# Optimization experiments

Measured on AMD Instinct MI355X. Metric: run time of the kernel, lower is better.

Reference implementation:

```python
import jax, jax.numpy as jnp
import numpy as np

B, L, D, H, T = 4, 1024, 1024, 16, 64


def cubic_interp_1d(vec, coords):
    # Catmull-Rom interpolation of 1D vec at real-valued coords (any shape).
    Lv = vec.shape[0]
    i = jnp.floor(coords).astype(jnp.int32)
    t = coords - i.astype(coords.dtype)
    im1 = jnp.clip(i - 1, 0, Lv - 1)
    i0 = jnp.clip(i, 0, Lv - 1)
    i1 = jnp.clip(i + 1, 0, Lv - 1)
    i2 = jnp.clip(i + 2, 0, Lv - 1)
    p0, p1, p2, p3 = vec[im1], vec[i0], vec[i1], vec[i2]
    t2 = t * t
    t3 = t2 * t
    return 0.5 * (2 * p1 + (-p0 + p2) * t + (2 * p0 - 5 * p1 + 4 * p2 - p3) * t2
                  + (-p0 + 3 * p1 - 3 * p2 + p3) * t3)


def linear_interp_1d(vec, coords):
    Lv = vec.shape[0]
    i = jnp.floor(coords).astype(jnp.int32)
    t = coords - i.astype(coords.dtype)
    i0 = jnp.clip(i, 0, Lv - 1)
    i1 = jnp.clip(i + 1, 0, Lv - 1)
    return vec[i0] * (1 - t) + vec[i1] * t


def setup_inputs() -> dict:
    key = jax.random.key(0)
    ks = jax.random.split(key, 12)
    s = 1.0 / np.sqrt(D)
    return {
        "x": jax.random.normal(ks[0], (B, L, D), jnp.float32),
        "t_enc": jax.random.normal(ks[1], (B, L, T), jnp.float32),
        "WQ": jax.random.normal(ks[2], (D, D), jnp.float32) * s,
        "WK": jax.random.normal(ks[3], (D, D), jnp.float32) * s,
        "WV": jax.random.normal(ks[4], (D, D), jnp.float32) * s,
        "WO": jax.random.normal(ks[5], (D, D), jnp.float32) * s,
        "bO": jnp.zeros((D,), jnp.float32),
        "Wt": jax.random.normal(ks[6], (T,), jnp.float32) * (1.0 / np.sqrt(T)),
        "bt": jnp.zeros((), jnp.float32),
        "p_mat": jax.random.normal(ks[7], (D, L), jnp.float32) * 0.02,
        "r_mat": jax.random.normal(ks[8], (D, L), jnp.float32) * 0.02,
        "alpha": jnp.ones((H,), jnp.float32),
        "beta": jnp.ones((H,), jnp.float32),
        "gamma": jnp.zeros((H,), jnp.float32),
    }


def reference(x, t_enc, WQ, WK, WV, WO, bO, Wt, bt, p_mat, r_mat, alpha, beta, gamma):
    Bx, Lx, Dx = x.shape
    d = Dx // H
    # projections: torch Linear y = x @ W.T
    Q = (x @ WQ.T).reshape(Bx, Lx, H, d).transpose(0, 2, 1, 3)  # [B,H,L,d]
    K = (x @ WK.T).reshape(Bx, Lx, H, d).transpose(0, 2, 1, 3)
    V = (x @ WV.T).reshape(Bx, Lx, H, d).transpose(0, 2, 1, 3)
    P = x.reshape(Bx, Lx, H, d).transpose(0, 2, 1, 3)
    # time-warped coordinates
    tau = jax.nn.sigmoid(t_enc @ Wt + bt)          # [B,L]
    coords = tau * (Lx - 1)
    # q_sca = cubic_interp(p_mat, coords).sum(-1); interp is linear in p_mat,
    # so interpolate the d-summed vector (same math, no [B,L,d] blowup).
    q_sca = cubic_interp_1d(p_mat.sum(0), coords)  # [B,L]
    delta = jnp.abs(coords[:, :, None] - coords[:, None, :])   # [B,L,L]
    r_sca = linear_interp_1d(r_mat.sum(0), delta)              # [B,L,L]
    qsum = q_sca[:, :, None] + q_sca[:, None, :]               # [B,L,L]
    Pij = jnp.einsum('bhid,bhjd->bhij', P, P)                  # [B,H,L,L]
    a = alpha[None, :, None, None]
    b = beta[None, :, None, None]
    c = gamma[None, :, None, None]
    S = a * qsum[:, None] + b * r_sca[:, None] + c
    scores = jnp.einsum('bhid,bhjd->bhij', Q, K) / jnp.sqrt(jnp.asarray(d, x.dtype)) + S * Pij
    attn = jax.nn.softmax(scores, axis=-1)
    out = jnp.einsum('bhij,bhjd->bhid', attn, V)
    out = out.transpose(0, 2, 1, 3).reshape(Bx, Lx, Dx)
    return out @ WO.T + bO
```

## Files before the change

kernel.cpp:

```cpp
#include <hip/hip_runtime.h>
#include <cstdint>
#include <cstddef>

typedef __attribute__((ext_vector_type(8))) short s8v;
typedef __attribute__((ext_vector_type(4))) float f32x4;

__device__ __forceinline__ unsigned short f2bf(float f) {
  unsigned int u = __builtin_bit_cast(unsigned int, f);
  unsigned int r = (u + 0x7fffu + ((u >> 16) & 1u)) >> 16;
  return (unsigned short)r;
}
__device__ __forceinline__ float bf2f(unsigned short s) {
  unsigned int u = ((unsigned int)s) << 16;
  return __builtin_bit_cast(float, u);
}

__device__ __forceinline__ void gload16(const void* g, void* l) {
  __builtin_amdgcn_global_load_lds(
      (const __attribute__((address_space(1))) void*)g,
      (__attribute__((address_space(3))) void*)l, 16, 0, 0);
}


__global__ __launch_bounds__(256)
void colsum_kernel(const float* __restrict__ p_mat, const float* __restrict__ r_mat,
                   float* __restrict__ q_vec, float* __restrict__ r_vec) {
  int col = blockIdx.x * 256 + threadIdx.x;
  int d0 = blockIdx.y * 32;
  float sp = 0.f, sr = 0.f;
  for (int d = d0; d < d0 + 32; ++d) {
    sp += p_mat[d * 1024 + col];
    sr += r_mat[d * 1024 + col];
  }
  atomicAdd(&q_vec[col], sp);
  atomicAdd(&r_vec[col], sr);
}

__global__ __launch_bounds__(256)
void coords_kernel(const float* __restrict__ t_enc, const float* __restrict__ Wt,
                   const float* __restrict__ bt, const float* __restrict__ q_vec,
                   float* __restrict__ coords, float* __restrict__ q_sca) {
  int item = blockIdx.x * 4 + (threadIdx.x >> 6);
  int lane = threadIdx.x & 63;
  float v = t_enc[(size_t)item * 64 + lane] * Wt[lane];
  v += __shfl_xor(v, 32);
  v += __shfl_xor(v, 16);
  v += __shfl_xor(v, 8);
  v += __shfl_xor(v, 4);
  v += __shfl_xor(v, 2);
  v += __shfl_xor(v, 1);
  if (lane == 0) {
    float z = v + bt[0];
    float tau = 1.0f / (1.0f + expf(-z));
    float c = tau * 1023.0f;
    coords[item] = c;
    float fi = floorf(c);
    int i = (int)fi;
    float t = c - fi;
    int im1 = i - 1; if (im1 < 0) im1 = 0; if (im1 > 1023) im1 = 1023;
    int i0 = i; if (i0 < 0) i0 = 0; if (i0 > 1023) i0 = 1023;
    int i1 = i + 1; if (i1 > 1023) i1 = 1023;
    int i2 = i + 2; if (i2 > 1023) i2 = 1023;
    float p0 = q_vec[im1], p1 = q_vec[i0], p2 = q_vec[i1], p3 = q_vec[i2];
    float t2 = t * t, t3 = t2 * t;
    q_sca[item] = 0.5f * (2.f * p1 + (-p0 + p2) * t +
                          (2.f * p0 - 5.f * p1 + 4.f * p2 - p3) * t2 +
                          (-p0 + 3.f * p1 - 3.f * p2 + p3) * t3);
  }
}

__global__ __launch_bounds__(256)
void conv_all_kernel(const float* __restrict__ x,
                     const float* __restrict__ w0, const float* __restrict__ w1,
                     const float* __restrict__ w2, const float* __restrict__ w3,
                     unsigned short* __restrict__ xb, unsigned short* __restrict__ xlo,
                     unsigned short* __restrict__ wb) {
  int bx = blockIdx.x;
  if (bx < 2048) {
    size_t i8 = ((size_t)bx * 256 + threadIdx.x) * 8;
    float4 a = *(const float4*)(x + i8);
    float4 b = *(const float4*)(x + i8 + 4);
    float v[8] = {a.x, a.y, a.z, a.w, b.x, b.y, b.z, b.w};
    s8v h, lo;
    #pragma unroll
    for (int j = 0; j < 8; ++j) {
      unsigned short hh = f2bf(v[j]);
      h[j] = (short)hh;
      lo[j] = (short)f2bf(v[j] - bf2f(hh));
    }
    *(s8v*)(xb + i8) = h;
    *(s8v*)(xlo + i8) = lo;
  } else {
    size_t i8 = ((size_t)(bx - 2048) * 256 + threadIdx.x) * 8;
    int sel = (int)(i8 >> 20);
    const float* w = (sel == 0) ? w0 : (sel == 1) ? w1 : (sel == 2) ? w2 : w3;
    size_t off = i8 & 0xFFFFF;
    float4 a = *(const float4*)(w + off);
    float4 b = *(const float4*)(w + off + 4);
    float v[8] = {a.x, a.y, a.z, a.w, b.x, b.y, b.z, b.w};
    s8v h;
    #pragma unroll
    for (int j = 0; j < 8; ++j) h[j] = (short)f2bf(v[j]);
    *(s8v*)(wb + i8) = h;
  }
}


__global__ __launch_bounds__(256, 2)
void gemm_qkv_kernel(const unsigned short* __restrict__ Abuf,
                     const unsigned short* __restrict__ Wb,
                     unsigned short* __restrict__ Qb,
                     unsigned short* __restrict__ Kb,
                     unsigned short* __restrict__ Vb) {
  __shared__ unsigned short As[2][128 * 64];
  __shared__ unsigned short Bs[2][128 * 64];
  const int tid = threadIdx.x, w = tid >> 6, l = tid & 63;
  const int sel = blockIdx.x >> 3;
  const int nb = (blockIdx.x & 7) * 128;
  const int m0 = blockIdx.y * 128;
  const unsigned short* Bbuf = Wb + ((size_t)sel << 20);
  const int wr = w >> 1, wc = w & 1;
  const int ll = l & 15, lg = l >> 4;
  const int cs = (((l & 7) ^ ((l >> 3) & 7)) * 8);

  const f32x4 zero4 = {0.f, 0.f, 0.f, 0.f};
  f32x4 acc[4][4];
  #pragma unroll
  for (int i = 0; i < 4; ++i) {
    #pragma unroll
    for (int j = 0; j < 4; ++j) acc[i][j] = zero4;
  }

  auto stage = [&](int kt, int buf) {
    #pragma unroll
    for (int q = 0; q < 4; ++q) {
      const int seg = w * 4 + q;
      const int row = seg * 8 + (l >> 3);
      const int col = kt * 64 + cs;
      gload16(Abuf + (size_t)(m0 + row) * 1024 + col, &As[buf][seg * 512 + l * 8]);
      gload16(Bbuf + (size_t)(nb + row) * 1024 + col, &Bs[buf][seg * 512 + l * 8]);
    }
  };

  stage(0, 0);
  for (int kt = 0; kt < 16; ++kt) {
    __syncthreads();
    if (kt < 15) stage(kt + 1, (kt + 1) & 1);
    const int bb = kt & 1;
    #pragma unroll
    for (int ks = 0; ks < 2; ++ks) {
      const int gsw = ((ks * 4 + lg) ^ (ll & 7)) * 8;
      s8v af[4], bf[4];
      #pragma unroll
      for (int mi = 0; mi < 4; ++mi)
        af[mi] = *(const s8v*)&As[bb][(wr * 64 + mi * 16 + ll) * 64 + gsw];
      #pragma unroll
      for (int ni = 0; ni < 4; ++ni)
        bf[ni] = *(const s8v*)&Bs[bb][(wc * 64 + ni * 16 + ll) * 64 + gsw];
      #pragma unroll
      for (int mi = 0; mi < 4; ++mi) {
        #pragma unroll
        for (int ni = 0; ni < 4; ++ni)
          acc[mi][ni] = __builtin_amdgcn_mfma_f32_16x16x32_bf16(af[mi], bf[ni], acc[mi][ni], 0, 0, 0);
      }
    }
  }

  unsigned short* dst = (sel == 0) ? Qb : ((sel == 1) ? Kb : Vb);
  unsigned short* ch = &As[0][0];
  const int err = tid >> 3;
  const int ecb = tid & 7;
  #pragma unroll
  for (int mi = 0; mi < 4; ++mi) {
    __syncthreads();
    #pragma unroll
    for (int ni = 0; ni < 4; ++ni) {
      #pragma unroll
      for (int r = 0; r < 4; ++r)
        ch[(wr * 16 + lg * 4 + r) * 136 + wc * 64 + ni * 16 + ll] = f2bf(acc[mi][ni][r]);
    }
    __syncthreads();
    int m = m0 + (err >> 4) * 64 + mi * 16 + (err & 15);
    int ncol = nb + ecb * 16;
    int bb2 = m >> 10, lr = m & 1023, hh = ncol >> 6, dd = ncol & 63;
    unsigned short* gp = &dst[(((size_t)bb2 * 16 + hh) * 1024 + lr) * 64 + dd];
    *(s8v*)(gp)     = *(const s8v*)&ch[err * 136 + ecb * 16];
    *(s8v*)(gp + 8) = *(const s8v*)&ch[err * 136 + ecb * 16 + 8];
  }
}


__global__ __launch_bounds__(256, 2)
void gemm_out_kernel(const unsigned short* __restrict__ Abuf,
                     const unsigned short* __restrict__ Bbuf,
                     const float* __restrict__ bO,
                     float* __restrict__ out) {
  __shared__ unsigned short As[2][128 * 64];
  __shared__ unsigned short Bs[2][128 * 64];
  const int tid = threadIdx.x, w = tid >> 6, l = tid & 63;
  const int nb = blockIdx.x * 128;
  const int m0 = blockIdx.y * 128;
  const int wr = w >> 1, wc = w & 1;
  const int ll = l & 15, lg = l >> 4;
  const int cs = (((l & 7) ^ ((l >> 3) & 7)) * 8);

  const f32x4 zero4 = {0.f, 0.f, 0.f, 0.f};
  f32x4 acc[4][4];
  #pragma unroll
  for (int i = 0; i < 4; ++i) {
    #pragma unroll
    for (int j = 0; j < 4; ++j) acc[i][j] = zero4;
  }

  auto stage = [&](int kt, int buf) {
    #pragma unroll
    for (int q = 0; q < 4; ++q) {
      const int seg = w * 4 + q;
      const int row = seg * 8 + (l >> 3);
      const int col = kt * 64 + cs;
      gload16(Abuf + (size_t)(m0 + row) * 1024 + col, &As[buf][seg * 512 + l * 8]);
      gload16(Bbuf + (size_t)(nb + row) * 1024 + col, &Bs[buf][seg * 512 + l * 8]);
    }
  };

  stage(0, 0);
  for (int kt = 0; kt < 16; ++kt) {
    __syncthreads();
    if (kt < 15) stage(kt + 1, (kt + 1) & 1);
    const int bb = kt & 1;
    #pragma unroll
    for (int ks = 0; ks < 2; ++ks) {
      const int gsw = ((ks * 4 + lg) ^ (ll & 7)) * 8;
      s8v af[4], bf[4];
      #pragma unroll
      for (int mi = 0; mi < 4; ++mi)
        af[mi] = *(const s8v*)&As[bb][(wr * 64 + mi * 16 + ll) * 64 + gsw];
      #pragma unroll
      for (int ni = 0; ni < 4; ++ni)
        bf[ni] = *(const s8v*)&Bs[bb][(wc * 64 + ni * 16 + ll) * 64 + gsw];
      #pragma unroll
      for (int mi = 0; mi < 4; ++mi) {
        #pragma unroll
        for (int ni = 0; ni < 4; ++ni)
          acc[mi][ni] = __builtin_amdgcn_mfma_f32_16x16x32_bf16(af[mi], bf[ni], acc[mi][ni], 0, 0, 0);
      }
    }
  }

  #pragma unroll
  for (int mi = 0; mi < 4; ++mi) {
    #pragma unroll
    for (int ni = 0; ni < 4; ++ni) {
      #pragma unroll
      for (int r = 0; r < 4; ++r) {
        int m = m0 + wr * 64 + mi * 16 + (l >> 4) * 4 + r;
        int ncol = nb + wc * 64 + ni * 16 + ll;
        out[(size_t)m * 1024 + ncol] = acc[mi][ni][r] + bO[ncol];
      }
    }
  }
}


__global__ __launch_bounds__(512, 2)
void attn_kernel(const unsigned short* __restrict__ Qb,
                 const unsigned short* __restrict__ Kb,
                 const unsigned short* __restrict__ Vb,
                 const unsigned short* __restrict__ xb,
                 const unsigned short* __restrict__ xlo,
                 const float* __restrict__ coords,
                 const float* __restrict__ q_sca,
                 const float* __restrict__ r_vec,
                 const float* __restrict__ alpha,
                 const float* __restrict__ beta,
                 const float* __restrict__ gamma,
                 unsigned short* __restrict__ AO) {
  __shared__ float2 rp_s[1024];
  __shared__ unsigned short Ks[2][64 * 64];
  __shared__ unsigned short Ph[2][64 * 64];
  __shared__ unsigned short Pl[2][64 * 64];
  __shared__ unsigned short Vt[64 * 64];
  __shared__ unsigned short pbuf[8][16 * 64];

  const int tid = threadIdx.x;
  const int w = tid >> 6;
  const int l = tid & 63;
  const int gid = blockIdx.x;
  const int bh = (gid & 7) * 8 + ((gid >> 3) >> 3);
  const int xt = (gid >> 3) & 7;
  const int b = bh >> 4;
  const int h = bh & 15;
  const int iw = xt * 128 + w * 16;

  for (int t = tid; t < 1024; t += 512) {
    float r0 = r_vec[t];
    float r1 = r_vec[t < 1023 ? t + 1 : 1023];
    rp_s[t] = make_float2(r0, r1);
  }

  const float INVLN2 = 1.4426950408889634f;
  const float a_h = alpha[h] * INVLN2, b_h = beta[h] * INVLN2, c_h = gamma[h] * INVLN2;
  const int lg = l >> 4;
  const int ll = l & 15;
  const int rowg = lg * 4;
  const int akg = lg * 8;

  float aqi[4], ci[4];
  #pragma unroll
  for (int r = 0; r < 4; ++r) {
    aqi[r] = fmaf(a_h, q_sca[b * 1024 + iw + rowg + r], c_h);
    ci[r] = coords[b * 1024 + iw + rowg + r];
  }

  s8v qf[2], pih[2], pil[2];
  {
    const unsigned short* qp = Qb + ((size_t)bh * 1024 + iw + ll) * 64 + akg;
    qf[0] = *(const s8v*)(qp);
    qf[1] = *(const s8v*)(qp + 32);
    const unsigned short* xp = xb + ((size_t)b * 1024 + iw + ll) * 1024 + h * 64 + akg;
    pih[0] = *(const s8v*)(xp);
    pih[1] = *(const s8v*)(xp + 32);
    const unsigned short* xq = xlo + ((size_t)b * 1024 + iw + ll) * 1024 + h * 64 + akg;
    pil[0] = *(const s8v*)(xq);
    pil[1] = *(const s8v*)(xq + 32);
  }

  const f32x4 zero4 = {0.f, 0.f, 0.f, 0.f};
  f32x4 o[4];
  #pragma unroll
  for (int ds = 0; ds < 4; ++ds) o[ds] = zero4;
  float mrow[4], lsum[4];
  #pragma unroll
  for (int r = 0; r < 4; ++r) { mrow[r] = -3.0e38f; lsum[r] = 0.f; }

  unsigned short* pw = pbuf[w];
  const int cs = (((l & 7) ^ ((l >> 3) & 7)) * 8);
  const int srow = l >> 3;

  auto stage = [&](int j0, int buf) {
    const int row = w * 8 + srow;
    gload16(Kb + ((size_t)bh * 1024 + j0 + row) * 64 + cs, &Ks[buf][w * 512 + l * 8]);
    gload16(xb + ((size_t)b * 1024 + j0 + row) * 1024 + h * 64 + cs, &Ph[buf][w * 512 + l * 8]);
    gload16(xlo + ((size_t)b * 1024 + j0 + row) * 1024 + h * 64 + cs, &Pl[buf][w * 512 + l * 8]);
  };
  auto vload = [&](int j0) -> s8v {
    return *(const s8v*)(Vb + ((size_t)bh * 1024 + j0 + l) * 64 + w * 8);
  };
  auto vwrite = [&](const s8v& vv) {
    #pragma unroll
    for (int e = 0; e < 8; ++e) {
      const int row = w * 8 + e;
      Vt[row * 64 + (((l >> 3) ^ (row & 7)) * 8) + (l & 7)] = (unsigned short)vv[e];
    }
  };

  stage(0, 0);
  s8v vv0 = vload(0);
  stage(64, 1);
  s8v vv1 = vload(64);
  vwrite(vv0);
  __syncthreads();

#define ATTN_TILE(T, PAR, VCONS, VPROD)                                          \
  {                                                                              \
    const int j0 = (T) * 64;                                                     \
    float cj[4], aqj[4];                                                         \
    _Pragma("unroll")                                                            \
    for (int s = 0; s < 4; ++s) {                                                \
      cj[s] = coords[b * 1024 + j0 + ll + 16 * s];                               \
      aqj[s] = a_h * q_sca[b * 1024 + j0 + ll + 16 * s];                         \
    }                                                                            \
    f32x4 aqk[4], app[4];                                                        \
    _Pragma("unroll")                                                            \
    for (int s = 0; s < 4; ++s) { aqk[s] = zero4; app[s] = zero4; }              \
    _Pragma("unroll")                                                            \
    for (int ks = 0; ks < 2; ++ks) {                                             \
      _Pragma("unroll")                                                          \
      for (int s = 0; s < 4; ++s) {                                              \
        const int rb = (ll + 16 * s) * 64 + (((ks * 4 + lg) ^ (ll & 7)) * 8);    \
        s8v kf = *(const s8v*)&Ks[PAR][rb];                                      \
        s8v hf = *(const s8v*)&Ph[PAR][rb];                                      \
        s8v lf = *(const s8v*)&Pl[PAR][rb];                                      \
        aqk[s] = __builtin_amdgcn_mfma_f32_16x16x32_bf16(qf[ks], kf, aqk[s], 0, 0, 0);   \
        app[s] = __builtin_amdgcn_mfma_f32_16x16x32_bf16(pih[ks], hf, app[s], 0, 0, 0);  \
        app[s] = __builtin_amdgcn_mfma_f32_16x16x32_bf16(pih[ks], lf, app[s], 0, 0, 0);  \
        app[s] = __builtin_amdgcn_mfma_f32_16x16x32_bf16(pil[ks], hf, app[s], 0, 0, 0);  \
      }                                                                          \
    }                                                                            \
    float tmax[4];                                                               \
    _Pragma("unroll")                                                            \
    for (int r = 0; r < 4; ++r) tmax[r] = -3.0e38f;                              \
    _Pragma("unroll")                                                            \
    for (int s = 0; s < 4; ++s) {                                                \
      _Pragma("unroll")                                                          \
      for (int r = 0; r < 4; ++r) {                                              \
        float delta = fabsf(ci[r] - cj[s]);                                      \
        int i0 = (int)delta;                                                     \
        float tt = delta - (float)i0;                                            \
        float2 rr = rp_s[i0];                                                    \
        float rs = fmaf(tt, rr.y - rr.x, rr.x);                                  \
        float S = fmaf(b_h, rs, aqi[r] + aqj[s]);                                \
        float v = fmaf(0.18033688f, aqk[s][r], S * app[s][r]);                   \
        app[s][r] = v;                                                           \
        tmax[r] = fmaxf(tmax[r], v);                                             \
      }                                                                          \
    }                                                                            \
    _Pragma("unroll")                                                            \
    for (int r = 0; r < 4; ++r) {                                                \
      float v = tmax[r];                                                         \
      v = fmaxf(v, __shfl_xor(v, 1));                                            \
      v = fmaxf(v, __shfl_xor(v, 2));                                            \
      v = fmaxf(v, __shfl_xor(v, 4));                                            \
      v = fmaxf(v, __shfl_xor(v, 8));                                            \
      float mn = fmaxf(mrow[r], v);                                              \
      float scale = exp2f(mrow[r] - mn);                                         \
      mrow[r] = mn;                                                              \
      lsum[r] *= scale;                                                          \
      o[0][r] *= scale; o[1][r] *= scale; o[2][r] *= scale; o[3][r] *= scale;    \
    }                                                                            \
    _Pragma("unroll")                                                            \
    for (int s = 0; s < 4; ++s) {                                                \
      const int pg = ((2 * s + (ll >> 3)));                                      \
      _Pragma("unroll")                                                          \
      for (int r = 0; r < 4; ++r) {                                              \
        float e = exp2f(app[s][r] - mrow[r]);                                    \
        lsum[r] += e;                                                            \
        const int row = rowg + r;                                                \
        pw[row * 64 + ((pg ^ (row & 7)) * 8) + (ll & 7)] =                       \
            (unsigned short)(__builtin_bit_cast(unsigned int, e) >> 16);         \
      }                                                                          \
    }                                                                            \
    _Pragma("unroll")                                                            \
    for (int ks = 0; ks < 2; ++ks) {                                             \
      s8v pa = *(const s8v*)&pw[ll * 64 + (((ks * 4 + lg) ^ (ll & 7)) * 8)];     \
      _Pragma("unroll")                                                          \
      for (int dq = 0; dq < 4; ++dq) {                                           \
        const int vrow = ll + 16 * dq;                                           \
        s8v vf = *(const s8v*)&Vt[vrow * 64 + (((ks * 4 + lg) ^ (ll & 7)) * 8)]; \
        o[dq] = __builtin_amdgcn_mfma_f32_16x16x32_bf16(pa, vf, o[dq], 0, 0, 0); \
      }                                                                          \
    }                                                                            \
    __syncthreads();                          \
    if ((T) < 15) {                                                              \
      vwrite(VCONS);                                           \
      if ((T) < 14) {                                                            \
        stage((T) + 2 > 15 ? 0 : ((T) + 2) * 64, PAR);                           \
        VPROD = vload(((T) + 2) * 64);                                           \
      }                                                                          \
      asm volatile("s_waitcnt lgkmcnt(0)" ::: "memory");                         \
      __builtin_amdgcn_sched_barrier(0);                                         \
      __builtin_amdgcn_s_barrier();                                              \
    }                                                                            \
  }

  for (int t2 = 0; t2 < 16; t2 += 2) {
    ATTN_TILE(t2, 0, vv1, vv0);
    ATTN_TILE(t2 + 1, 1, vv0, vv1);
  }
#undef ATTN_TILE

  #pragma unroll
  for (int r = 0; r < 4; ++r) {
    float v = lsum[r];
    v += __shfl_xor(v, 1);
    v += __shfl_xor(v, 2);
    v += __shfl_xor(v, 4);
    v += __shfl_xor(v, 8);
    lsum[r] = 1.0f / v;
  }
  #pragma unroll
  for (int ds = 0; ds < 4; ++ds) {
    #pragma unroll
    for (int r = 0; r < 4; ++r) {
      AO[((size_t)b * 1024 + iw + rowg + r) * 1024 + h * 64 + ll + 16 * ds] =
          f2bf(o[ds][r] * lsum[r]);
    }
  }
}


extern "C" void kernel_launch(void* const* d_in, const int* in_sizes, int n_in,
                              void* d_out, int out_size, void* d_ws, size_t ws_size,
                              hipStream_t stream) {
  const float* x     = (const float*)d_in[0];
  const float* t_enc = (const float*)d_in[1];
  const float* WQ    = (const float*)d_in[2];
  const float* WK    = (const float*)d_in[3];
  const float* WV    = (const float*)d_in[4];
  const float* WO    = (const float*)d_in[5];
  const float* bO    = (const float*)d_in[6];
  const float* Wt    = (const float*)d_in[7];
  const float* bt    = (const float*)d_in[8];
  const float* p_mat = (const float*)d_in[9];
  const float* r_mat = (const float*)d_in[10];
  const float* alpha = (const float*)d_in[11];
  const float* beta  = (const float*)d_in[12];
  const float* gamma = (const float*)d_in[13];
  float* out = (float*)d_out;

  char* ws = (char*)d_ws;
  unsigned short* xb  = (unsigned short*)(ws + ((size_t)0 << 20));
  unsigned short* xlo = (unsigned short*)(ws + ((size_t)8 << 20));
  unsigned short* wb  = (unsigned short*)(ws + ((size_t)16 << 20));
  unsigned short* Qb  = (unsigned short*)(ws + ((size_t)24 << 20));
  unsigned short* Kb  = (unsigned short*)(ws + ((size_t)32 << 20));
  unsigned short* Vb  = (unsigned short*)(ws + ((size_t)40 << 20));
  unsigned short* AO  = (unsigned short*)(ws + ((size_t)48 << 20));
  float* q_vec  = (float*)(ws + ((size_t)56 << 20));
  float* r_vec  = q_vec + 1024;
  float* coords = r_vec + 1024;
  float* q_sca  = coords + 4096;

  hipMemsetAsync(q_vec, 0, 2048 * sizeof(float), stream);
  colsum_kernel<<<dim3(4, 32), 256, 0, stream>>>(p_mat, r_mat, q_vec, r_vec);
  coords_kernel<<<1024, 256, 0, stream>>>(t_enc, Wt, bt, q_vec, coords, q_sca);
  conv_all_kernel<<<4096, 256, 0, stream>>>(x, WQ, WK, WV, WO, xb, xlo, wb);
  gemm_qkv_kernel<<<dim3(24, 32), 256, 0, stream>>>(xb, wb, Qb, Kb, Vb);
  attn_kernel<<<512, 512, 0, stream>>>(Qb, Kb, Vb, xb, xlo, coords, q_sca,
                                       r_vec, alpha, beta, gamma, AO);
  gemm_out_kernel<<<dim3(8, 32), 256, 0, stream>>>(AO, wb + ((size_t)3 << 20), bO, out);
}
```

Before: 267.7 us.

## Double-buffer V tile and split P·V into halves to drop a barrier

Result: slower. 273.9 us (+2.3%).

```diff
diff --git a/kernel.cpp b/kernel.cpp
--- a/kernel.cpp
+++ b/kernel.cpp
@@ -279,8 +279,8 @@
   __shared__ unsigned short Ks[2][64 * 64];
   __shared__ unsigned short Ph[2][64 * 64];
   __shared__ unsigned short Pl[2][64 * 64];
-  __shared__ unsigned short Vt[64 * 64];
-  __shared__ unsigned short pbuf[8][16 * 64];
+  __shared__ unsigned short Vt[2][64 * 64];
+  __shared__ unsigned short pbuf[8][16 * 32];
 
   const int tid = threadIdx.x;
   const int w = tid >> 6;
@@ -346,11 +346,11 @@
   auto vload = [&](int j0) -> s8v {
     return *(const s8v*)(Vb + ((size_t)bh * 1024 + j0 + l) * 64 + w * 8);
   };
-  auto vwrite = [&](const s8v& vv) {
+  auto vwrite = [&](const s8v& vv, int vb) {
     #pragma unroll
     for (int e = 0; e < 8; ++e) {
       const int row = w * 8 + e;
-      Vt[row * 64 + (((l >> 3) ^ (row & 7)) * 8) + (l & 7)] = (unsigned short)vv[e];
+      Vt[vb][row * 64 + (((l >> 3) ^ (row & 7)) * 8) + (l & 7)] = (unsigned short)vv[e];
     }
   };
 
@@ -358,12 +358,13 @@
   s8v vv0 = vload(0);
   stage(64, 1);
   s8v vv1 = vload(64);
-  vwrite(vv0);
+  vwrite(vv0, 0);
   __syncthreads();
 
 #define ATTN_TILE(T, PAR, VCONS, VPROD)                                          \
   {                                                                              \
     const int j0 = (T) * 64;                                                     \
+    const int VB = (T) & 1;                                                      \
     float cj[4], aqj[4];                                                         \
     _Pragma("unroll")                                                            \
     for (int s = 0; s < 4; ++s) {                                                \
@@ -418,39 +419,42 @@
       lsum[r] *= scale;                                                          \
       o[0][r] *= scale; o[1][r] *= scale; o[2][r] *= scale; o[3][r] *= scale;    \
     }                                                                            \
-    _Pragma("unroll")                                                            \
-    for (int s = 0; s < 4; ++s) {                                                \
-      const int pg = ((2 * s + (ll >> 3)));                                      \
+           \
+    _Pragma("unroll")                                                            \
+    for (int h2 = 0; h2 < 2; ++h2) {                                             \
       _Pragma("unroll")                                                          \
-      for (int r = 0; r < 4; ++r) {                                              \
-        float e = exp2f(app[s][r] - mrow[r]);                                    \
-        lsum[r] += e;                                                            \
-        const int row = rowg + r;                                                \
-        pw[row * 64 + ((pg ^ (row & 7)) * 8) + (ll & 7)] =                       \
-            (unsigned short)(__builtin_bit_cast(unsigned int, e) >> 16);         \
+      for (int s2 = 0; s2 < 2; ++s2) {                                           \
+        const int s = h2 * 2 + s2;                                               \
+        const int cg = (ll >> 3) + s2 * 2;                                       \
+        _Pragma("unroll")                                                        \
+        for (int r = 0; r < 4; ++r) {                                            \
+          float e = exp2f(app[s][r] - mrow[r]);                                  \
+          lsum[r] += e;                                                          \
+          const int row = rowg + r;                                              \
+          pw[row * 32 + ((cg ^ (row & 3)) * 8) + (ll & 7)] =                     \
+              (unsigned short)(__builtin_bit_cast(unsigned int, e) >> 16);       \
+        }                                                                        \
+      }                                                                          \
+      __builtin_amdgcn_sched_barrier(0);                                         \
+      {                                                                          \
+        s8v pa = *(const s8v*)&pw[ll * 32 + ((lg ^ (ll & 3)) * 8)];              \
+        _Pragma("unroll")                                                        \
+        for (int dq = 0; dq < 4; ++dq) {                                         \
+          const int vrow = ll + 16 * dq;                                         \
+          s8v vf = *(const s8v*)&Vt[VB][vrow * 64 + (((h2 * 4 + lg) ^ (ll & 7)) * 8)]; \
+          o[dq] = __builtin_amdgcn_mfma_f32_16x16x32_bf16(pa, vf, o[dq], 0, 0, 0);     \
+        }                                                                        \
+      }                                                                          \
+      __builtin_amdgcn_sched_barrier(0);                                         \
+    }                                                                            \
+    if ((T) < 15) {                                                              \
+      vwrite(VCONS, VB ^ 1);                          \
+      if ((T) < 14) {                                                            \
+        stage(((T) + 2) * 64, PAR);                                              \
+        VPROD = vload(((T) + 2) * 64);                                           \
       }                                                                          \
     }                                                                            \
-    _Pragma("unroll")                                                            \
-    for (int ks = 0; ks < 2; ++ks) {                                             \
-      s8v pa = *(const s8v*)&pw[ll * 64 + (((ks * 4 + lg) ^ (ll & 7)) * 8)];     \
-      _Pragma("unroll")                                                          \
-      for (int dq = 0; dq < 4; ++dq) {                                           \
-        const int vrow = ll + 16 * dq;                                           \
-        s8v vf = *(const s8v*)&Vt[vrow * 64 + (((ks * 4 + lg) ^ (ll & 7)) * 8)]; \
-        o[dq] = __builtin_amdgcn_mfma_f32_16x16x32_bf16(pa, vf, o[dq], 0, 0, 0); \
-      }                                                                          \
-    }                                                                            \
-    __syncthreads();                          \
-    if ((T) < 15) {                                                              \
-      vwrite(VCONS);                                           \
-      if ((T) < 14) {                                                            \
-        stage((T) + 2 > 15 ? 0 : ((T) + 2) * 64, PAR);                           \
-        VPROD = vload(((T) + 2) * 64);                                           \
-      }                                                                          \
-      asm volatile("s_waitcnt lgkmcnt(0)" ::: "memory");                         \
-      __builtin_amdgcn_sched_barrier(0);                                         \
-      __builtin_amdgcn_s_barrier();                                              \
-    }                                                                            \
+    __syncthreads();                                \
   }
 
   for (int t2 = 0; t2 < 16; t2 += 2) {
```
